# Kernel optimization log

Measured on AMD Instinct MI355X. Metric: run time of the kernel, lower is better.

Reference implementation:

```python
import jax, jax.numpy as jnp
import numpy as np

N, E, T, B = 10000, 80000, 240000, 32
HF, EMB = 256, 64
EDGE_BINS, ANG_BINS = 80, 40
N_CONV = 12  # 4 alignn layers x 2 EGGC + 4 gcn EGGC


def layernorm(x, scale, bias):
    m = x.mean(-1, keepdims=True)
    v = ((x - m) ** 2).mean(-1, keepdims=True)
    return (x - m) / jnp.sqrt(v + 1e-5) * scale + bias


def mlp_layer(x, W, b, ln):
    # Linear -> LayerNorm -> SiLU
    return jax.nn.silu(layernorm(x @ W + b, ln[0], ln[1]))


def rbf(x, vmin, vmax, bins):
    centers = jnp.linspace(vmin, vmax, bins)
    gamma = 0.5 / ((vmax - vmin) / bins) ** 2
    return jnp.exp(-gamma * (x[..., None] - centers) ** 2)


def eggc(W, b, ln_s, ln_b, src, dst, h, e, n_nodes):
    """Edge-gated graph conv. W:[5,F,F] b:[5,F] order: src_gate,dst_gate,edge_gate,src_update,dst_update.
    ln_s/ln_b:[2,F] order: edges, nodes."""
    e_src = h @ W[0] + b[0]
    e_dst = h @ W[1] + b[1]
    sigma = jax.nn.sigmoid(e_src[src] + e_dst[dst] + e @ W[2] + b[2])  # [n_edges, F]
    e_out = layernorm(sigma * e, ln_s[0], ln_b[0])
    Bh = h @ W[4] + b[4]  # dst_update
    sum_sh = jax.ops.segment_sum(Bh[src] * sigma, dst, num_segments=n_nodes)
    sum_s = jax.ops.segment_sum(sigma, dst, num_segments=n_nodes)
    h_out = h @ W[3] + b[3] + sum_sh / (sum_s + 1e-8)  # src_update + gated mean
    return layernorm(h_out, ln_s[1], ln_b[1]), e_out


def setup_inputs() -> dict:
    key = jax.random.key(0)
    ks = jax.random.split(key, 24)
    rn = lambda k, shp: (jax.random.normal(k, shp, dtype=jnp.float32) * 0.05)
    ln_init = lambda f: jnp.stack([jnp.ones((f,), jnp.float32), jnp.zeros((f,), jnp.float32)])
    inp = {
        'atom_features': jax.random.normal(ks[0], (N, 92), dtype=jnp.float32),
        'bondlength': jax.random.uniform(ks[1], (E,), dtype=jnp.float32) * 8.0,
        'angle_h': jax.random.uniform(ks[2], (T,), dtype=jnp.float32) * 2.0 - 1.0,
        'src': jax.random.randint(ks[3], (E,), 0, N, dtype=jnp.int32),
        'dst': jax.random.randint(ks[4], (E,), 0, N, dtype=jnp.int32),
        'lg_src': jax.random.randint(ks[5], (T,), 0, E, dtype=jnp.int32),
        'lg_dst': jax.random.randint(ks[6], (T,), 0, E, dtype=jnp.int32),
        'graph_ids': jnp.sort(jax.random.randint(ks[7], (N,), 0, B)).astype(jnp.int32),
        'atom_W': rn(ks[8], (92, HF)), 'atom_b': jnp.zeros((HF,), jnp.float32), 'atom_ln': ln_init(HF),
        'edge_W1': rn(ks[9], (EDGE_BINS, EMB)), 'edge_b1': jnp.zeros((EMB,), jnp.float32), 'edge_ln1': ln_init(EMB),
        'edge_W2': rn(ks[10], (EMB, HF)), 'edge_b2': jnp.zeros((HF,), jnp.float32), 'edge_ln2': ln_init(HF),
        'ang_W1': rn(ks[11], (ANG_BINS, EMB)), 'ang_b1': jnp.zeros((EMB,), jnp.float32), 'ang_ln1': ln_init(EMB),
        'ang_W2': rn(ks[12], (EMB, HF)), 'ang_b2': jnp.zeros((HF,), jnp.float32), 'ang_ln2': ln_init(HF),
        'conv_W': rn(ks[13], (N_CONV, 5, HF, HF)),
        'conv_b': jnp.zeros((N_CONV, 5, HF), jnp.float32),
        'conv_ln_s': jnp.ones((N_CONV, 2, HF), jnp.float32),
        'conv_ln_b': jnp.zeros((N_CONV, 2, HF), jnp.float32),
    }
    return inp


def reference(atom_features, bondlength, angle_h, src, dst, lg_src, lg_dst, graph_ids,
              atom_W, atom_b, atom_ln, edge_W1, edge_b1, edge_ln1, edge_W2, edge_b2, edge_ln2,
              ang_W1, ang_b1, ang_ln1, ang_W2, ang_b2, ang_ln2,
              conv_W, conv_b, conv_ln_s, conv_ln_b):
    n_nodes = atom_features.shape[0]
    n_edges = bondlength.shape[0]
    # embeddings
    z = mlp_layer(mlp_layer(rbf(angle_h, -1.0, 1.0, ANG_BINS), ang_W1, ang_b1, ang_ln1), ang_W2, ang_b2, ang_ln2)
    x = mlp_layer(atom_features, atom_W, atom_b, atom_ln)
    y = mlp_layer(mlp_layer(rbf(bondlength, 0.0, 8.0, EDGE_BINS), edge_W1, edge_b1, edge_ln1), edge_W2, edge_b2, edge_ln2)
    # 4 ALIGNN layers: edge_update on line graph, then node_update on graph
    for i in range(4):
        j = 2 * i
        y, z = eggc(conv_W[j], conv_b[j], conv_ln_s[j], conv_ln_b[j], lg_src, lg_dst, y, z, n_edges)
        j = 2 * i + 1
        x, y = eggc(conv_W[j], conv_b[j], conv_ln_s[j], conv_ln_b[j], src, dst, x, y, n_nodes)
    # 4 GCN layers
    for i in range(4):
        j = 8 + i
        x, y = eggc(conv_W[j], conv_b[j], conv_ln_s[j], conv_ln_b[j], src, dst, x, y, n_nodes)
    # AvgPooling readout per graph
    sums = jax.ops.segment_sum(x, graph_ids, num_segments=B)
    counts = jax.ops.segment_sum(jnp.ones((n_nodes,), x.dtype), graph_ids, num_segments=B)
    return sums / jnp.maximum(counts, 1.0)[:, None]
```

## Files before the change

### kernel.cpp

```cpp
#include <hip/hip_runtime.h>
#include <hip/hip_bf16.h>

typedef unsigned short u16;
typedef unsigned int u32;
typedef __attribute__((ext_vector_type(8))) short short8;
typedef __attribute__((ext_vector_type(4))) float f32x4;

__device__ __forceinline__ float bf2f(u16 u) { return __uint_as_float(((u32)u) << 16); }
__device__ __forceinline__ u16 f2bf(float f) {
  u32 x = __float_as_uint(f);
  return (u16)((x + 0x7FFFu + ((x >> 16) & 1u)) >> 16);
}
__device__ __forceinline__ void up4(uint2 r, float* o) {
  o[0] = bf2f((u16)(r.x & 0xFFFF)); o[1] = bf2f((u16)(r.x >> 16));
  o[2] = bf2f((u16)(r.y & 0xFFFF)); o[3] = bf2f((u16)(r.y >> 16));
}
__device__ __forceinline__ uint2 pk4(const float* o) {
  uint2 r;
  r.x = (u32)f2bf(o[0]) | ((u32)f2bf(o[1]) << 16);
  r.y = (u32)f2bf(o[2]) | ((u32)f2bf(o[3]) << 16);
  return r;
}
__device__ __forceinline__ float wsum64(float v) {
#pragma unroll
  for (int o = 32; o > 0; o >>= 1) v += __shfl_xor(v, o, 64);
  return v;
}
__device__ __forceinline__ float sigm(float x) { return 1.0f / (1.0f + __expf(-x)); }

__global__ __launch_bounds__(256) void fill_kernel(float* __restrict__ out, int n, float v) {
  int i = blockIdx.x * 256 + threadIdx.x;
  if (i < n) out[i] = v;
}

__global__ __launch_bounds__(256) void wtrans(const float* __restrict__ in,
                                              u16* __restrict__ out, int R, int Ccols) {
  __shared__ float t[64][65];
  const float* ip = in + (size_t)blockIdx.z * R * Ccols;
  u16* op = out + (size_t)blockIdx.z * R * Ccols;
  int kb = blockIdx.x * 64, nb = blockIdx.y * 64;
  int lr = threadIdx.x >> 4, lc = (threadIdx.x & 15) * 4;
#pragma unroll
  for (int p = 0; p < 4; ++p) {
    int k = lr + p * 16;
    float4 v = *(const float4*)(ip + (size_t)(kb + k) * Ccols + nb + lc);
    t[k][lc + 0] = v.x; t[k][lc + 1] = v.y; t[k][lc + 2] = v.z; t[k][lc + 3] = v.w;
  }
  __syncthreads();
#pragma unroll
  for (int p = 0; p < 4; ++p) {
    int n = lr + p * 16;
    uint2 pk;
    pk.x = (u32)f2bf(t[lc + 0][n]) | ((u32)f2bf(t[lc + 1][n]) << 16);
    pk.y = (u32)f2bf(t[lc + 2][n]) | ((u32)f2bf(t[lc + 3][n]) << 16);
    *(uint2*)(op + (size_t)(nb + n) * R + kb + lc) = pk;
  }
}

__global__ __launch_bounds__(256) void csr_hist(const int* __restrict__ dst,
                                                int* __restrict__ hist, int ne) {
  int e = blockIdx.x * 256 + threadIdx.x;
  if (e < ne) atomicAdd(&hist[dst[e]], 1);
}
__global__ __launch_bounds__(1024) void scan1(const int* __restrict__ in,
                                              int* __restrict__ out1, int* __restrict__ bsum, int n) {
  __shared__ int s[1024];
  int i = blockIdx.x * 1024 + threadIdx.x;
  int v = (i < n) ? in[i] : 0;
  s[threadIdx.x] = v; __syncthreads();
  for (int off = 1; off < 1024; off <<= 1) {
    int t = (threadIdx.x >= (u32)off) ? s[threadIdx.x - off] : 0;
    __syncthreads();
    s[threadIdx.x] += t;
    __syncthreads();
  }
  if (i < n) out1[i] = s[threadIdx.x];
  if (threadIdx.x == 1023) bsum[blockIdx.x] = s[1023];
}
__global__ __launch_bounds__(128) void scan2(int* __restrict__ bsum, int nb) {
  __shared__ int s[128];
  int v = (threadIdx.x < (u32)nb) ? bsum[threadIdx.x] : 0;
  s[threadIdx.x] = v; __syncthreads();
  for (int off = 1; off < 128; off <<= 1) {
    int t = (threadIdx.x >= (u32)off) ? s[threadIdx.x - off] : 0;
    __syncthreads();
    s[threadIdx.x] += t;
    __syncthreads();
  }
  if (threadIdx.x < (u32)nb) bsum[threadIdx.x] = threadIdx.x ? s[threadIdx.x - 1] : 0;
}
__global__ __launch_bounds__(256) void scan3(int* __restrict__ offs,
                                             const int* __restrict__ bsum, int n) {
  int i = blockIdx.x * 256 + threadIdx.x;
  if (i == 0) offs[0] = 0;
  if (i < n) offs[1 + i] += bsum[i >> 10];
}
__global__ __launch_bounds__(256) void csr_scatter(const int* __restrict__ dst,
                                                   int* __restrict__ cursor,
                                                   const int* __restrict__ offs,
                                                   int* __restrict__ eid, int ne) {
  int e = blockIdx.x * 256 + threadIdx.x;
  if (e < ne) {
    int d = dst[e];
    int p = offs[d] + atomicAdd(&cursor[d], 1);
    eid[p] = e;
  }
}
__global__ __launch_bounds__(256) void inv_perm(const int* __restrict__ eid,
                                                int* __restrict__ pos, int n) {
  int i = blockIdx.x * 256 + threadIdx.x;
  if (i < n) pos[eid[i]] = i;
}
__global__ __launch_bounds__(256) void remap_k(const int* __restrict__ idx,
                                               const int* __restrict__ map,
                                               int* __restrict__ out, int n) {
  int i = blockIdx.x * 256 + threadIdx.x;
  if (i < n) out[i] = map[idx[i]];
}
__global__ __launch_bounds__(256) void compose_src(const int* __restrict__ eid,
                                                   const int* __restrict__ srcv,
                                                   const int* __restrict__ map,
                                                   int* __restrict__ out, int n) {
  int i = blockIdx.x * 256 + threadIdx.x;
  if (i < n) {
    int s = srcv[eid[i]];
    out[i] = map ? map[s] : s;
  }
}

__global__ __launch_bounds__(256) void embed_s1(
    const float* __restrict__ xin, const float* __restrict__ W1,
    const float* __restrict__ b1, const float* __restrict__ ln1,
    u16* __restrict__ t1, int rows, int bins, float vmin, float vmax,
    const int* __restrict__ perm) {
  int row = (blockIdx.x * 256 + threadIdx.x) >> 6;
  if (row >= rows) return;
  int lane = threadIdx.x & 63;
  float xv = xin[row];
  float rng = vmax - vmin;
  float step = rng / (float)(bins - 1);
  float gamma = 0.5f * ((float)bins / rng) * ((float)bins / rng);
  float rb = 0.f, rb2 = 0.f;
  if (lane < bins) {
    float d = xv - (vmin + lane * step);
    rb = __expf(-gamma * d * d);
  }
  if (bins > 64 && lane < bins - 64) {
    float d = xv - (vmin + (lane + 64) * step);
    rb2 = __expf(-gamma * d * d);
  }
  float u = b1[lane];
  int k1 = bins < 64 ? bins : 64;
  for (int k = 0; k < k1; ++k) {
    float rv = __shfl(rb, k, 64);
    u = fmaf(rv, W1[k * 64 + lane], u);
  }
  for (int k = 64; k < bins; ++k) {
    float rv = __shfl(rb2, k - 64, 64);
    u = fmaf(rv, W1[k * 64 + lane], u);
  }
  float s = wsum64(u), s2 = wsum64(u * u);
  float m = s * (1.f / 64.f), var = s2 * (1.f / 64.f) - m * m;
  float t = (u - m) * rsqrtf(var + 1e-5f) * ln1[lane] + ln1[64 + lane];
  int orow = perm ? perm[row] : row;
  t1[(size_t)orow * 64 + lane] = f2bf(t * sigm(t));
}

__global__ __launch_bounds__(256) void ln_silu(u16* __restrict__ buf,
                                               const float* __restrict__ ln, int rows) {
  int row = (blockIdx.x * 256 + threadIdx.x) >> 6;
  if (row >= rows) return;
  int lane = threadIdx.x & 63;
  int f = lane * 4;
  float v[4];
  up4(*(const uint2*)(buf + (size_t)row * 256 + f), v);
  float s = wsum64(v[0] + v[1] + v[2] + v[3]);
  float s2 = wsum64(v[0] * v[0] + v[1] * v[1] + v[2] * v[2] + v[3] * v[3]);
  float m = s * (1.f / 256.f);
  float rs = rsqrtf(s2 * (1.f / 256.f) - m * m + 1e-5f);
  float o[4];
#pragma unroll
  for (int k = 0; k < 4; ++k) {
    float t = (v[k] - m) * rs * ln[f + k] + ln[256 + f + k];
    o[k] = t * sigm(t);
  }
  *(uint2*)(buf + (size_t)row * 256 + f) = pk4(o);
}

__global__ __launch_bounds__(256) void atom_embed_kernel(
    const float* __restrict__ af, const float* __restrict__ W,
    const float* __restrict__ b, const float* __restrict__ ln,
    u16* __restrict__ out, int rows) {
  int row = blockIdx.x;
  if (row >= rows) return;
  __shared__ float a_s[92];
  __shared__ float red[8];
  int tid = threadIdx.x;
  if (tid < 92) a_s[tid] = af[(size_t)row * 92 + tid];
  __syncthreads();
  float v = b[tid];
#pragma unroll 4
  for (int k = 0; k < 92; ++k) v = fmaf(a_s[k], W[k * 256 + tid], v);
  float s = wsum64(v), s2 = wsum64(v * v);
  int lane = tid & 63, wid = tid >> 6;
  if (lane == 0) { red[wid] = s; red[4 + wid] = s2; }
  __syncthreads();
  s = red[0] + red[1] + red[2] + red[3];
  s2 = red[4] + red[5] + red[6] + red[7];
  float m = s * (1.f / 256.f), var = s2 * (1.f / 256.f) - m * m;
  float t = (v - m) * rsqrtf(var + 1e-5f) * ln[tid] + ln[256 + tid];
  out[(size_t)row * 256 + tid] = f2bf(t * sigm(t));
}

__global__ __launch_bounds__(256) void mfma_gemm(
    const u16* __restrict__ A, const u16* __restrict__ Wt,
    const float* __restrict__ bias, u16* __restrict__ C,
    int M, int K, int ldc, int slab_step) {
  int bm = blockIdx.x * 128;
  if (bm >= M) return;
  int bn = blockIdx.y * 128;
  int slab = (bn >> 8) * slab_step;
  const u16* Wp = Wt + (size_t)slab * 256 * K + (size_t)(bn & 255) * K;
  const float* bp = bias + slab * 256 + (bn & 255);
  int tid = threadIdx.x;
  int w = tid >> 6, lane = tid & 63;
  int q = lane >> 4, r = lane & 15;
  int m0 = (w & 1) * 64;
  int n0 = (w >> 1) * 64;
  const u16* aptr[4];
#pragma unroll
  for (int mi = 0; mi < 4; ++mi) {
    int m = bm + m0 + mi * 16 + r;
    m = m < M - 1 ? m : M - 1;
    aptr[mi] = A + (size_t)m * K + q * 8;
  }
  const u16* wptr[4];
#pragma unroll
  for (int ni = 0; ni < 4; ++ni)
    wptr[ni] = Wp + (size_t)(n0 + ni * 16 + r) * K + q * 8;
  f32x4 acc[4][4] = {};
  for (int kb = 0; kb < K; kb += 32) {
    short8 bfr[4], afr[4];
#pragma unroll
    for (int mi = 0; mi < 4; ++mi) bfr[mi] = *(const short8*)(aptr[mi] + kb);
#pragma unroll
    for (int ni = 0; ni < 4; ++ni) afr[ni] = *(const short8*)(wptr[ni] + kb);
#pragma unroll
    for (int mi = 0; mi < 4; ++mi)
#pragma unroll
      for (int ni = 0; ni < 4; ++ni)
        acc[mi][ni] = __builtin_amdgcn_mfma_f32_16x16x32_bf16(afr[ni], bfr[mi],
                                                              acc[mi][ni], 0, 0, 0);
  }
#pragma unroll
  for (int mi = 0; mi < 4; ++mi) {
    int m = bm + m0 + mi * 16 + r;
    if (m < M) {
#pragma unroll
      for (int ni = 0; ni < 4; ++ni) {
        int n = n0 + ni * 16 + q * 4;
        float4 bv = *(const float4*)(bp + n);
        uint2 o;
        o.x = (u32)f2bf(acc[mi][ni].x + bv.x) | ((u32)f2bf(acc[mi][ni].y + bv.y) << 16);
        o.y = (u32)f2bf(acc[mi][ni].z + bv.z) | ((u32)f2bf(acc[mi][ni].w + bv.w) << 16);
        *(uint2*)(C + (size_t)m * ldc + bn + n) = o;
      }
    }
  }
}

__global__ __launch_bounds__(512) void mega_eggc(
    u16* __restrict__ h, u16* __restrict__ e,
    const u16* __restrict__ G0Bh,
    const u16* __restrict__ Wt13, const float* __restrict__ b13,
    const u16* __restrict__ Wt2, const float* __restrict__ b2v,
    const int* __restrict__ src_perm, const int* __restrict__ offs,
    const float* __restrict__ lnS, const float* __restrict__ lnB, int nn) {
  __shared__ u16 g1ah[16][520];
  __shared__ u16 pe[64][264];
  int tid = threadIdx.x;
  int w = tid >> 6, lane = tid & 63;
  int q = lane >> 4, r = lane & 15;
  int v0 = blockIdx.x * 16;

  {
    int mrow = v0 + r; if (mrow > nn - 1) mrow = nn - 1;
    const u16* arow = h + (size_t)mrow * 256 + q * 8;
    f32x4 acc[4] = {};
    for (int kb = 0; kb < 256; kb += 32) {
      short8 af = *(const short8*)(arow + kb);
#pragma unroll
      for (int t = 0; t < 4; ++t) {
        int ng = (4 * w + t) * 16 + r;
        const u16* wrow = Wt13 + (size_t)(ng >> 8) * 2 * 65536 +
                          (size_t)(ng & 255) * 256 + q * 8;
        short8 wf = *(const short8*)(wrow + kb);
        acc[t] = __builtin_amdgcn_mfma_f32_16x16x32_bf16(wf, af, acc[t], 0, 0, 0);
      }
    }
#pragma unroll
    for (int t = 0; t < 4; ++t) {
      int nb = (4 * w + t) * 16 + q * 4;
      const float* bp = b13 + (nb >> 8) * 2 * 256 + (nb & 255);
      float o[4] = {acc[t].x + bp[0], acc[t].y + bp[1], acc[t].z + bp[2], acc[t].w + bp[3]};
      *(uint2*)&g1ah[r][nb] = pk4(o);
    }
  }
  __syncthreads();

  int f = lane * 4;
  int r0 = offs[v0];
  int vend = v0 + 16 < nn ? v0 + 16 : nn;
  int r1 = offs[vend];
  int vA = v0 + w * 2, vB = vA + 1;
  int eA0 = vA < nn ? offs[vA] : 0, eA1 = vA < nn ? offs[vA + 1] : 0;
  int eB0 = vB < nn ? offs[vB] : 0, eB1 = vB < nn ? offs[vB + 1] : 0;
  float sshA[4] = {0, 0, 0, 0}, ssmA[4] = {0, 0, 0, 0};
  float sshB[4] = {0, 0, 0, 0}, ssmB[4] = {0, 0, 0, 0};
  float lwe[4], lbe[4];
#pragma unroll
  for (int k = 0; k < 4; ++k) { lwe[k] = lnS[f + k]; lbe[k] = lnB[f + k]; }

  for (int ec = r0; ec < r1; ec += 64) {
    {
      const u16* w0p = Wt2 + (size_t)((2 * w) * 16 + r) * 256 + q * 8;
      const u16* w1p = Wt2 + (size_t)((2 * w + 1) * 16 + r) * 256 + q * 8;
      f32x4 acc[4][2] = {};
      for (int kb = 0; kb < 256; kb += 32) {
        short8 wf0 = *(const short8*)(w0p + kb);
        short8 wf1 = *(const short8*)(w1p + kb);
#pragma unroll
        for (int mt = 0; mt < 4; ++mt) {
          int erow = ec + mt * 16 + r;
          if (erow > r1 - 1) erow = r1 - 1;
          short8 af = *(const short8*)(e + (size_t)erow * 256 + kb + q * 8);
          acc[mt][0] = __builtin_amdgcn_mfma_f32_16x16x32_bf16(wf0, af, acc[mt][0], 0, 0, 0);
          acc[mt][1] = __builtin_amdgcn_mfma_f32_16x16x32_bf16(wf1, af, acc[mt][1], 0, 0, 0);
        }
      }
#pragma unroll
      for (int mt = 0; mt < 4; ++mt)
#pragma unroll
        for (int nt = 0; nt < 2; ++nt) {
          int nb = (2 * w + nt) * 16 + q * 4;
          float o[4] = {acc[mt][nt].x + b2v[nb], acc[mt][nt].y + b2v[nb + 1],
                        acc[mt][nt].z + b2v[nb + 2], acc[mt][nt].w + b2v[nb + 3]};
          *(uint2*)&pe[mt * 16 + r][nb] = pk4(o);
        }
    }
    __syncthreads();
    int ce = ec + 64 < r1 ? ec + 64 : r1;
#pragma unroll
    for (int jj = 0; jj < 2; ++jj) {
      int vv = jj ? vB : vA;
      int i0 = jj ? eB0 : eA0, i1 = jj ? eB1 : eA1;
      int lo = i0 > ec ? i0 : ec, hi = i1 < ce ? i1 : ce;
      for (int i = lo; i < hi; ++i) {
        int sv = src_perm[i];
        float g0[4], bh[4], pv[4], ev[4], g1v[4];
        up4(*(const uint2*)(G0Bh + (size_t)sv * 512 + f), g0);
        up4(*(const uint2*)(G0Bh + (size_t)sv * 512 + 256 + f), bh);
        up4(*(const uint2*)&pe[i - ec][f], pv);
        up4(*(const uint2*)(e + (size_t)i * 256 + f), ev);
        up4(*(const uint2*)&g1ah[vv - v0][f], g1v);
        float t[4];
        float ssum = 0.f, s2sum = 0.f;
#pragma unroll
        for (int k = 0; k < 4; ++k) {
          float sg = sigm(g0[k] + g1v[k] + pv[k]);
          t[k] = sg * ev[k];
          if (jj) { sshB[k] = fmaf(bh[k], sg, sshB[k]); ssmB[k] += sg; }
          else    { sshA[k] = fmaf(bh[k], sg, sshA[k]); ssmA[k] += sg; }
          ssum += t[k]; s2sum += t[k] * t[k];
        }
        float s1 = wsum64(ssum), s2 = wsum64(s2sum);
        float mn = s1 * (1.f / 256.f);
        float rs = rsqrtf(s2 * (1.f / 256.f) - mn * mn + 1e-5f);
        float o[4];
#pragma unroll
        for (int k = 0; k < 4; ++k) o[k] = (t[k] - mn) * rs * lwe[k] + lbe[k];
        *(uint2*)(e + (size_t)i * 256 + f) = pk4(o);
      }
    }
    __syncthreads();
  }
#pragma unroll
  for (int jj = 0; jj < 2; ++jj) {
    int vv = jj ? vB : vA;
    if (vv < nn) {
      float ah[4], tt[4];
      up4(*(const uint2*)&g1ah[vv - v0][256 + f], ah);
      float ssum = 0.f, s2sum = 0.f;
#pragma unroll
      for (int k = 0; k < 4; ++k) {
        float sh = jj ? sshB[k] : sshA[k];
        float sm = jj ? ssmB[k] : ssmA[k];
        tt[k] = ah[k] + sh / (sm + 1e-8f);
        ssum += tt[k]; s2sum += tt[k] * tt[k];
      }
      float s1 = wsum64(ssum), s2 = wsum64(s2sum);
      float mn = s1 * (1.f / 256.f);
      float rs = rsqrtf(s2 * (1.f / 256.f) - mn * mn + 1e-5f);
      float o[4];
#pragma unroll
      for (int k = 0; k < 4; ++k)
        o[k] = (tt[k] - mn) * rs * lnS[256 + f + k] + lnB[256 + f + k];
      *(uint2*)(h + (size_t)vv * 256 + f) = pk4(o);
    }
  }
}

__global__ __launch_bounds__(256) void pool_acc(
    const u16* __restrict__ x, const int* __restrict__ gid,
    float* __restrict__ out, float* __restrict__ cnt, int n) {
  int v = (blockIdx.x * 256 + threadIdx.x) >> 6;
  if (v >= n) return;
  int lane = threadIdx.x & 63;
  int f = lane * 4;
  int g = gid[v];
  float xv[4];
  up4(*(const uint2*)(x + (size_t)v * 256 + f), xv);
  float* p = out + (size_t)g * 256 + f;
  unsafeAtomicAdd(p + 0, xv[0]);
  unsafeAtomicAdd(p + 1, xv[1]);
  unsafeAtomicAdd(p + 2, xv[2]);
  unsafeAtomicAdd(p + 3, xv[3]);
  if (lane == 0) unsafeAtomicAdd(cnt + g, 1.0f);
}
__global__ __launch_bounds__(256) void pool_div(float* __restrict__ out,
                                                const float* __restrict__ cnt, int n) {
  int i = blockIdx.x * blockDim.x + threadIdx.x;
  if (i < n) out[i] /= fmaxf(cnt[i >> 8], 1.0f);
}

extern "C" void kernel_launch(void* const* d_in, const int* in_sizes, int n_in,
                              void* d_out, int out_size, void* d_ws, size_t ws_size,
                              hipStream_t stream) {
  const float* atom_features = (const float*)d_in[0];
  const float* bondlength    = (const float*)d_in[1];
  const float* angle_h       = (const float*)d_in[2];
  const int*   src           = (const int*)d_in[3];
  const int*   dst           = (const int*)d_in[4];
  const int*   lg_src        = (const int*)d_in[5];
  const int*   lg_dst        = (const int*)d_in[6];
  const int*   gid           = (const int*)d_in[7];
  const float* atom_W  = (const float*)d_in[8];
  const float* atom_b  = (const float*)d_in[9];
  const float* atom_ln = (const float*)d_in[10];
  const float* edge_W1 = (const float*)d_in[11];
  const float* edge_b1 = (const float*)d_in[12];
  const float* edge_ln1= (const float*)d_in[13];
  const float* edge_W2 = (const float*)d_in[14];
  const float* edge_b2 = (const float*)d_in[15];
  const float* edge_ln2= (const float*)d_in[16];
  const float* ang_W1  = (const float*)d_in[17];
  const float* ang_b1  = (const float*)d_in[18];
  const float* ang_ln1 = (const float*)d_in[19];
  const float* ang_W2  = (const float*)d_in[20];
  const float* ang_b2  = (const float*)d_in[21];
  const float* ang_ln2 = (const float*)d_in[22];
  const float* conv_W  = (const float*)d_in[23];
  const float* conv_b  = (const float*)d_in[24];
  const float* conv_lns= (const float*)d_in[25];
  const float* conv_lnb= (const float*)d_in[26];

  int N = in_sizes[0] / 92;
  int E = in_sizes[1];
  int T = in_sizes[2];

  char* ws = (char*)d_ws;
  size_t o = 0;
  auto alloc = [&](size_t bytes) { size_t r = o; o = (o + bytes + 255) & ~(size_t)255; return r; };
  u16* z     = (u16*)(ws + alloc((size_t)T * 512));
  u16* y     = (u16*)(ws + alloc((size_t)E * 512));
  u16* x     = (u16*)(ws + alloc((size_t)N * 512));
  int* offsL = (int*)(ws + alloc((size_t)(E + 1) * 4));
  int* offsA = (int*)(ws + alloc((size_t)(N + 1) * 4));
  int* spL   = (int*)(ws + alloc((size_t)T * 4));
  int* spA   = (int*)(ws + alloc((size_t)E * 4));
  int* pA    = (int*)(ws + alloc((size_t)E * 4));
  int* pL    = (int*)(ws + alloc((size_t)T * 4));
  int* eidL  = (int*)(ws + alloc((size_t)T * 4));
  int* eidA  = (int*)(ws + alloc((size_t)E * 4));
  int* ldSt  = (int*)(ws + alloc((size_t)T * 4));
  int* tmp   = (int*)(ws + alloc((size_t)(E > N ? E : N) * 4));
  int* bsum  = (int*)(ws + alloc(1024));
  float* cnt = (float*)(ws + alloc(1024));
  u16* WtAll = (u16*)(ws + alloc((size_t)12 * 5 * 65536 * 2));
  u16* WtAng = (u16*)(ws + alloc((size_t)16384 * 2));
  u16* WtEdg = (u16*)(ws + alloc((size_t)16384 * 2));
  size_t scratch_base = o;
  size_t need = scratch_base + (size_t)E * 1024;
  {
    size_t embed_need = scratch_base + ((size_t)T + E) * 128;
    if (embed_need > need) need = embed_need;
  }
  if (ws_size < need) {
    fill_kernel<<<(out_size + 255) / 256, 256, 0, stream>>>(
        (float*)d_out, out_size, (float)(ws_size >> 20));
    return;
  }

  wtrans<<<dim3(4, 4, 60), 256, 0, stream>>>(conv_W, WtAll, 256, 256);
  wtrans<<<dim3(1, 4, 1), 256, 0, stream>>>(ang_W2, WtAng, 64, 256);
  wtrans<<<dim3(1, 4, 1), 256, 0, stream>>>(edge_W2, WtEdg, 64, 256);

  auto build_csr = [&](const int* dvec, int ne_, int nn_, int* offs_, int* eid_) {
    hipMemsetAsync(tmp, 0, (size_t)nn_ * 4, stream);
    csr_hist<<<(ne_ + 255) / 256, 256, 0, stream>>>(dvec, tmp, ne_);
    int nb = (nn_ + 1023) / 1024;
    scan1<<<nb, 1024, 0, stream>>>(tmp, offs_ + 1, bsum, nn_);
    scan2<<<1, 128, 0, stream>>>(bsum, nb);
    scan3<<<(nn_ + 255) / 256, 256, 0, stream>>>(offs_, bsum, nn_);
    hipMemsetAsync(tmp, 0, (size_t)nn_ * 4, stream);
    csr_scatter<<<(ne_ + 255) / 256, 256, 0, stream>>>(dvec, tmp, offs_, eid_, ne_);
  };
  build_csr(dst, E, N, offsA, eidA);
  inv_perm<<<(E + 255) / 256, 256, 0, stream>>>(eidA, pA, E);
  compose_src<<<(E + 255) / 256, 256, 0, stream>>>(eidA, src, nullptr, spA, E);
  remap_k<<<(T + 255) / 256, 256, 0, stream>>>(lg_dst, pA, ldSt, T);
  build_csr(ldSt, T, E, offsL, eidL);
  inv_perm<<<(T + 255) / 256, 256, 0, stream>>>(eidL, pL, T);
  compose_src<<<(T + 255) / 256, 256, 0, stream>>>(eidL, lg_src, pA, spL, T);

  u16* t1T = (u16*)(ws + scratch_base);
  u16* t1E = t1T + (size_t)T * 64;
  embed_s1<<<(T + 3) / 4, 256, 0, stream>>>(angle_h, ang_W1, ang_b1, ang_ln1,
                                            t1T, T, 40, -1.f, 1.f, pL);
  embed_s1<<<(E + 3) / 4, 256, 0, stream>>>(bondlength, edge_W1, edge_b1, edge_ln1,
                                            t1E, E, 80, 0.f, 8.f, pA);
  mfma_gemm<<<dim3((T + 127) / 128, 2), 256, 0, stream>>>(
      t1T, WtAng, ang_b2, z, T, 64, 256, 1);
  mfma_gemm<<<dim3((E + 127) / 128, 2), 256, 0, stream>>>(
      t1E, WtEdg, edge_b2, y, E, 64, 256, 1);
  ln_silu<<<(T + 3) / 4, 256, 0, stream>>>(z, ang_ln2, T);
  ln_silu<<<(E + 3) / 4, 256, 0, stream>>>(y, edge_ln2, E);
  atom_embed_kernel<<<N, 256, 0, stream>>>(atom_features, atom_W, atom_b, atom_ln, x, N);

  u16* G0Bh = (u16*)(ws + scratch_base);
  for (int l = 0; l < 12; ++l) {
    const u16* WtL  = WtAll + (size_t)l * 5 * 65536;
    const float* bl = conv_b + (size_t)l * 5 * 256;
    const float* lnS = conv_lns + (size_t)l * 512;
    const float* lnB = conv_lnb + (size_t)l * 512;
    bool line = (l < 8) && ((l & 1) == 0);
    u16* h = line ? y : x;
    u16* e = line ? z : y;
    const int* sperm = line ? spL : spA;
    const int* offs  = line ? offsL : offsA;
    int nn = line ? E : N;

    mfma_gemm<<<dim3((nn + 127) / 128, 4), 256, 0, stream>>>(
        h, WtL, bl, G0Bh, nn, 256, 512, 4);
    mega_eggc<<<(nn + 15) / 16, 512, 0, stream>>>(
        h, e, G0Bh, WtL + 65536, bl + 256, WtL + 2 * 65536, bl + 2 * 256,
        sperm, offs, lnS, lnB, nn);
  }

  hipMemsetAsync(d_out, 0, (size_t)out_size * sizeof(float), stream);
  hipMemsetAsync(cnt, 0, 256 * sizeof(float), stream);
  pool_acc<<<(N + 3) / 4, 256, 0, stream>>>(x, gid, (float*)d_out, cnt, N);
  pool_div<<<(out_size + 255) / 256, 256, 0, stream>>>((float*)d_out, cnt, out_size);
}
```

Before: 5.469 ms.

## Split EGGC kernel into line/atom variants with prefetched edge gathers

For atom-graph layers, all four node-side projections are computed in one wider GEMM through a slab map, so the fused kernel no longer recomputes the dst-gate and src-update MFMA per block. Both fused kernels now cache CSR offsets in shared memory and load each node's gate row into registers once. The per-edge loop interleaves the two nodes a wave owns and prefetches the next edge's gathered rows to hide memory latency. The cost is more register pressure, and a larger scratch write for the atom layers.

```diff
diff --git a/kernel.cpp b/kernel.cpp
--- a/kernel.cpp
+++ b/kernel.cpp
@@ -215,11 +215,11 @@
 __global__ __launch_bounds__(256) void mfma_gemm(
     const u16* __restrict__ A, const u16* __restrict__ Wt,
     const float* __restrict__ bias, u16* __restrict__ C,
-    int M, int K, int ldc, int slab_step) {
+    int M, int K, int ldc, u32 smap) {
   int bm = blockIdx.x * 128;
   if (bm >= M) return;
   int bn = blockIdx.y * 128;
-  int slab = (bn >> 8) * slab_step;
+  int slab = (smap >> ((bn >> 8) * 8)) & 0xFF;
   const u16* Wp = Wt + (size_t)slab * 256 * K + (size_t)(bn & 255) * K;
   const float* bp = bias + slab * 256 + (bn & 255);
   int tid = threadIdx.x;
@@ -269,20 +269,20 @@
   }
 }
 
-__global__ __launch_bounds__(512) void mega_eggc(
-    u16* __restrict__ h, u16* __restrict__ e,
-    const u16* __restrict__ G0Bh,
+__global__ __launch_bounds__(512) void mega_line(
+    u16* __restrict__ h, u16* __restrict__ e, const u16* __restrict__ G0Bh,
     const u16* __restrict__ Wt13, const float* __restrict__ b13,
     const u16* __restrict__ Wt2, const float* __restrict__ b2v,
     const int* __restrict__ src_perm, const int* __restrict__ offs,
     const float* __restrict__ lnS, const float* __restrict__ lnB, int nn) {
   __shared__ u16 g1ah[16][520];
   __shared__ u16 pe[64][264];
+  __shared__ int oloc[17];
   int tid = threadIdx.x;
   int w = tid >> 6, lane = tid & 63;
   int q = lane >> 4, r = lane & 15;
   int v0 = blockIdx.x * 16;
-
+  if (tid < 17) { int v = v0 + tid; oloc[tid] = offs[v < nn ? v : nn]; }
   {
     int mrow = v0 + r; if (mrow > nn - 1) mrow = nn - 1;
     const u16* arow = h + (size_t)mrow * 256 + q * 8;
@@ -307,19 +307,17 @@
     }
   }
   __syncthreads();
-
   int f = lane * 4;
-  int r0 = offs[v0];
-  int vend = v0 + 16 < nn ? v0 + 16 : nn;
-  int r1 = offs[vend];
-  int vA = v0 + w * 2, vB = vA + 1;
-  int eA0 = vA < nn ? offs[vA] : 0, eA1 = vA < nn ? offs[vA + 1] : 0;
-  int eB0 = vB < nn ? offs[vB] : 0, eB1 = vB < nn ? offs[vB + 1] : 0;
-  float sshA[4] = {0, 0, 0, 0}, ssmA[4] = {0, 0, 0, 0};
-  float sshB[4] = {0, 0, 0, 0}, ssmB[4] = {0, 0, 0, 0};
+  int r0 = oloc[0], r1 = oloc[16];
+  int eA0 = oloc[2 * w], eA1 = oloc[2 * w + 1];
+  int eB0 = oloc[2 * w + 1], eB1 = oloc[2 * w + 2];
+  float sshA[4] = {}, ssmA[4] = {}, sshB[4] = {}, ssmB[4] = {};
   float lwe[4], lbe[4];
 #pragma unroll
   for (int k = 0; k < 4; ++k) { lwe[k] = lnS[f + k]; lbe[k] = lnB[f + k]; }
+  float g1A[4], g1Bv[4];
+  up4(*(const uint2*)&g1ah[2 * w][f], g1A);
+  up4(*(const uint2*)&g1ah[2 * w + 1][f], g1Bv);
 
   for (int ec = r0; ec < r1; ec += 64) {
     {
@@ -349,47 +347,255 @@
         }
     }
     __syncthreads();
-    int ce = ec + 64 < r1 ? ec + 64 : r1;
-#pragma unroll
-    for (int jj = 0; jj < 2; ++jj) {
-      int vv = jj ? vB : vA;
-      int i0 = jj ? eB0 : eA0, i1 = jj ? eB1 : eA1;
-      int lo = i0 > ec ? i0 : ec, hi = i1 < ce ? i1 : ce;
-      for (int i = lo; i < hi; ++i) {
-        int sv = src_perm[i];
-        float g0[4], bh[4], pv[4], ev[4], g1v[4];
-        up4(*(const uint2*)(G0Bh + (size_t)sv * 512 + f), g0);
-        up4(*(const uint2*)(G0Bh + (size_t)sv * 512 + 256 + f), bh);
-        up4(*(const uint2*)&pe[i - ec][f], pv);
-        up4(*(const uint2*)(e + (size_t)i * 256 + f), ev);
-        up4(*(const uint2*)&g1ah[vv - v0][f], g1v);
-        float t[4];
-        float ssum = 0.f, s2sum = 0.f;
-#pragma unroll
-        for (int k = 0; k < 4; ++k) {
-          float sg = sigm(g0[k] + g1v[k] + pv[k]);
-          t[k] = sg * ev[k];
-          if (jj) { sshB[k] = fmaf(bh[k], sg, sshB[k]); ssmB[k] += sg; }
-          else    { sshA[k] = fmaf(bh[k], sg, sshA[k]); ssmA[k] += sg; }
-          ssum += t[k]; s2sum += t[k] * t[k];
-        }
-        float s1 = wsum64(ssum), s2 = wsum64(s2sum);
-        float mn = s1 * (1.f / 256.f);
-        float rs = rsqrtf(s2 * (1.f / 256.f) - mn * mn + 1e-5f);
-        float o[4];
-#pragma unroll
-        for (int k = 0; k < 4; ++k) o[k] = (t[k] - mn) * rs * lwe[k] + lbe[k];
-        *(uint2*)(e + (size_t)i * 256 + f) = pk4(o);
+    {
+      int ce = ec + 64 < r1 ? ec + 64 : r1;
+      int ia = eA0 > ec ? eA0 : ec, iaE = eA1 < ce ? eA1 : ce;
+      int ib = eB0 > ec ? eB0 : ec, ibE = eB1 < ce ? eB1 : ce;
+      uint2 ag0, abh, aev, bg0, bbh, bev;
+      if (ia < iaE) {
+        int sv = src_perm[ia];
+        ag0 = *(const uint2*)(G0Bh + (size_t)sv * 512 + f);
+        abh = *(const uint2*)(G0Bh + (size_t)sv * 512 + 256 + f);
+        aev = *(const uint2*)(e + (size_t)ia * 256 + f);
+      }
+      if (ib < ibE) {
+        int sv = src_perm[ib];
+        bg0 = *(const uint2*)(G0Bh + (size_t)sv * 512 + f);
+        bbh = *(const uint2*)(G0Bh + (size_t)sv * 512 + 256 + f);
+        bev = *(const uint2*)(e + (size_t)ib * 256 + f);
+      }
+      while (ia < iaE || ib < ibE) {
+        uint2 nag0, nabh, naev, nbg0, nbbh, nbev;
+        if (ia + 1 < iaE) {
+          int sv = src_perm[ia + 1];
+          nag0 = *(const uint2*)(G0Bh + (size_t)sv * 512 + f);
+          nabh = *(const uint2*)(G0Bh + (size_t)sv * 512 + 256 + f);
+          naev = *(const uint2*)(e + (size_t)(ia + 1) * 256 + f);
+        }
+        if (ib + 1 < ibE) {
+          int sv = src_perm[ib + 1];
+          nbg0 = *(const uint2*)(G0Bh + (size_t)sv * 512 + f);
+          nbbh = *(const uint2*)(G0Bh + (size_t)sv * 512 + 256 + f);
+          nbev = *(const uint2*)(e + (size_t)(ib + 1) * 256 + f);
+        }
+        if (ia < iaE) {
+          float g0v[4], bhv[4], pv[4], ev[4], t[4];
+          up4(ag0, g0v); up4(abh, bhv); up4(aev, ev);
+          up4(*(const uint2*)&pe[ia - ec][f], pv);
+          float ssum = 0.f, s2sum = 0.f;
+#pragma unroll
+          for (int k = 0; k < 4; ++k) {
+            float sg = sigm(g0v[k] + g1A[k] + pv[k]);
+            t[k] = sg * ev[k];
+            sshA[k] = fmaf(bhv[k], sg, sshA[k]);
+            ssmA[k] += sg;
+            ssum += t[k]; s2sum += t[k] * t[k];
+          }
+          float s1 = wsum64(ssum), s2 = wsum64(s2sum);
+          float mn = s1 * (1.f / 256.f);
+          float rs = rsqrtf(s2 * (1.f / 256.f) - mn * mn + 1e-5f);
+          float o[4];
+#pragma unroll
+          for (int k = 0; k < 4; ++k) o[k] = (t[k] - mn) * rs * lwe[k] + lbe[k];
+          *(uint2*)(e + (size_t)ia * 256 + f) = pk4(o);
+        }
+        if (ib < ibE) {
+          float g0v[4], bhv[4], pv[4], ev[4], t[4];
+          up4(bg0, g0v); up4(bbh, bhv); up4(bev, ev);
+          up4(*(const uint2*)&pe[ib - ec][f], pv);
+          float ssum = 0.f, s2sum = 0.f;
+#pragma unroll
+          for (int k = 0; k < 4; ++k) {
+            float sg = sigm(g0v[k] + g1Bv[k] + pv[k]);
+            t[k] = sg * ev[k];
+            sshB[k] = fmaf(bhv[k], sg, sshB[k]);
+            ssmB[k] += sg;
+            ssum += t[k]; s2sum += t[k] * t[k];
+          }
+          float s1 = wsum64(ssum), s2 = wsum64(s2sum);
+          float mn = s1 * (1.f / 256.f);
+          float rs = rsqrtf(s2 * (1.f / 256.f) - mn * mn + 1e-5f);
+          float o[4];
+#pragma unroll
+          for (int k = 0; k < 4; ++k) o[k] = (t[k] - mn) * rs * lwe[k] + lbe[k];
+          *(uint2*)(e + (size_t)ib * 256 + f) = pk4(o);
+        }
+        ag0 = nag0; abh = nabh; aev = naev;
+        bg0 = nbg0; bbh = nbbh; bev = nbev;
+        ia += (ia < iaE) ? 1 : 0;
+        ib += (ib < ibE) ? 1 : 0;
       }
     }
     __syncthreads();
   }
 #pragma unroll
   for (int jj = 0; jj < 2; ++jj) {
-    int vv = jj ? vB : vA;
+    int vv = v0 + 2 * w + jj;
     if (vv < nn) {
       float ah[4], tt[4];
-      up4(*(const uint2*)&g1ah[vv - v0][256 + f], ah);
+      up4(*(const uint2*)&g1ah[2 * w + jj][256 + f], ah);
+      float ssum = 0.f, s2sum = 0.f;
+#pragma unroll
+      for (int k = 0; k < 4; ++k) {
+        float sh = jj ? sshB[k] : sshA[k];
+        float sm = jj ? ssmB[k] : ssmA[k];
+        tt[k] = ah[k] + sh / (sm + 1e-8f);
+        ssum += tt[k]; s2sum += tt[k] * tt[k];
+      }
+      float s1 = wsum64(ssum), s2 = wsum64(s2sum);
+      float mn = s1 * (1.f / 256.f);
+      float rs = rsqrtf(s2 * (1.f / 256.f) - mn * mn + 1e-5f);
+      float o[4];
+#pragma unroll
+      for (int k = 0; k < 4; ++k)
+        o[k] = (tt[k] - mn) * rs * lnS[256 + f + k] + lnB[256 + f + k];
+      *(uint2*)(h + (size_t)vv * 256 + f) = pk4(o);
+    }
+  }
+}
+
+__global__ __launch_bounds__(512) void mega_atom(
+    u16* __restrict__ h, u16* __restrict__ e, const u16* __restrict__ GAll,
+    const u16* __restrict__ Wt2, const float* __restrict__ b2v,
+    const int* __restrict__ src_perm, const int* __restrict__ offs,
+    const float* __restrict__ lnS, const float* __restrict__ lnB, int nn) {
+  __shared__ u16 pe[64][264];
+  __shared__ int oloc[17];
+  int tid = threadIdx.x;
+  int w = tid >> 6, lane = tid & 63;
+  int q = lane >> 4, r = lane & 15;
+  int v0 = blockIdx.x * 16;
+  if (tid < 17) { int v = v0 + tid; oloc[tid] = offs[v < nn ? v : nn]; }
+  __syncthreads();
+  int f = lane * 4;
+  int r0 = oloc[0], r1 = oloc[16];
+  int eA0 = oloc[2 * w], eA1 = oloc[2 * w + 1];
+  int eB0 = oloc[2 * w + 1], eB1 = oloc[2 * w + 2];
+  float sshA[4] = {}, ssmA[4] = {}, sshB[4] = {}, ssmB[4] = {};
+  float lwe[4], lbe[4];
+#pragma unroll
+  for (int k = 0; k < 4; ++k) { lwe[k] = lnS[f + k]; lbe[k] = lnB[f + k]; }
+  int vAc = v0 + 2 * w;     if (vAc > nn - 1) vAc = nn - 1;
+  int vBc = v0 + 2 * w + 1; if (vBc > nn - 1) vBc = nn - 1;
+  float g1A[4], g1Bv[4];
+  up4(*(const uint2*)(GAll + (size_t)vAc * 1024 + 256 + f), g1A);
+  up4(*(const uint2*)(GAll + (size_t)vBc * 1024 + 256 + f), g1Bv);
+
+  for (int ec = r0; ec < r1; ec += 64) {
+    {
+      const u16* w0p = Wt2 + (size_t)((2 * w) * 16 + r) * 256 + q * 8;
+      const u16* w1p = Wt2 + (size_t)((2 * w + 1) * 16 + r) * 256 + q * 8;
+      f32x4 acc[4][2] = {};
+      for (int kb = 0; kb < 256; kb += 32) {
+        short8 wf0 = *(const short8*)(w0p + kb);
+        short8 wf1 = *(const short8*)(w1p + kb);
+#pragma unroll
+        for (int mt = 0; mt < 4; ++mt) {
+          int erow = ec + mt * 16 + r;
+          if (erow > r1 - 1) erow = r1 - 1;
+          short8 af = *(const short8*)(e + (size_t)erow * 256 + kb + q * 8);
+          acc[mt][0] = __builtin_amdgcn_mfma_f32_16x16x32_bf16(wf0, af, acc[mt][0], 0, 0, 0);
+          acc[mt][1] = __builtin_amdgcn_mfma_f32_16x16x32_bf16(wf1, af, acc[mt][1], 0, 0, 0);
+        }
+      }
+#pragma unroll
+      for (int mt = 0; mt < 4; ++mt)
+#pragma unroll
+        for (int nt = 0; nt < 2; ++nt) {
+          int nb = (2 * w + nt) * 16 + q * 4;
+          float o[4] = {acc[mt][nt].x + b2v[nb], acc[mt][nt].y + b2v[nb + 1],
+                        acc[mt][nt].z + b2v[nb + 2], acc[mt][nt].w + b2v[nb + 3]};
+          *(uint2*)&pe[mt * 16 + r][nb] = pk4(o);
+        }
+    }
+    __syncthreads();
+    {
+      int ce = ec + 64 < r1 ? ec + 64 : r1;
+      int ia = eA0 > ec ? eA0 : ec, iaE = eA1 < ce ? eA1 : ce;
+      int ib = eB0 > ec ? eB0 : ec, ibE = eB1 < ce ? eB1 : ce;
+      uint2 ag0, abh, aev, bg0, bbh, bev;
+      if (ia < iaE) {
+        int sv = src_perm[ia];
+        ag0 = *(const uint2*)(GAll + (size_t)sv * 1024 + f);
+        abh = *(const uint2*)(GAll + (size_t)sv * 1024 + 768 + f);
+        aev = *(const uint2*)(e + (size_t)ia * 256 + f);
+      }
+      if (ib < ibE) {
+        int sv = src_perm[ib];
+        bg0 = *(const uint2*)(GAll + (size_t)sv * 1024 + f);
+        bbh = *(const uint2*)(GAll + (size_t)sv * 1024 + 768 + f);
+        bev = *(const uint2*)(e + (size_t)ib * 256 + f);
+      }
+      while (ia < iaE || ib < ibE) {
+        uint2 nag0, nabh, naev, nbg0, nbbh, nbev;
+        if (ia + 1 < iaE) {
+          int sv = src_perm[ia + 1];
+          nag0 = *(const uint2*)(GAll + (size_t)sv * 1024 + f);
+          nabh = *(const uint2*)(GAll + (size_t)sv * 1024 + 768 + f);
+          naev = *(const uint2*)(e + (size_t)(ia + 1) * 256 + f);
+        }
+        if (ib + 1 < ibE) {
+          int sv = src_perm[ib + 1];
+          nbg0 = *(const uint2*)(GAll + (size_t)sv * 1024 + f);
+          nbbh = *(const uint2*)(GAll + (size_t)sv * 1024 + 768 + f);
+          nbev = *(const uint2*)(e + (size_t)(ib + 1) * 256 + f);
+        }
+        if (ia < iaE) {
+          float g0v[4], bhv[4], pv[4], ev[4], t[4];
+          up4(ag0, g0v); up4(abh, bhv); up4(aev, ev);
+          up4(*(const uint2*)&pe[ia - ec][f], pv);
+          float ssum = 0.f, s2sum = 0.f;
+#pragma unroll
+          for (int k = 0; k < 4; ++k) {
+            float sg = sigm(g0v[k] + g1A[k] + pv[k]);
+            t[k] = sg * ev[k];
+            sshA[k] = fmaf(bhv[k], sg, sshA[k]);
+            ssmA[k] += sg;
+            ssum += t[k]; s2sum += t[k] * t[k];
+          }
+          float s1 = wsum64(ssum), s2 = wsum64(s2sum);
+          float mn = s1 * (1.f / 256.f);
+          float rs = rsqrtf(s2 * (1.f / 256.f) - mn * mn + 1e-5f);
+          float o[4];
+#pragma unroll
+          for (int k = 0; k < 4; ++k) o[k] = (t[k] - mn) * rs * lwe[k] + lbe[k];
+          *(uint2*)(e + (size_t)ia * 256 + f) = pk4(o);
+        }
+        if (ib < ibE) {
+          float g0v[4], bhv[4], pv[4], ev[4], t[4];
+          up4(bg0, g0v); up4(bbh, bhv); up4(bev, ev);
+          up4(*(const uint2*)&pe[ib - ec][f], pv);
+          float ssum = 0.f, s2sum = 0.f;
+#pragma unroll
+          for (int k = 0; k < 4; ++k) {
+            float sg = sigm(g0v[k] + g1Bv[k] + pv[k]);
+            t[k] = sg * ev[k];
+            sshB[k] = fmaf(bhv[k], sg, sshB[k]);
+            ssmB[k] += sg;
+            ssum += t[k]; s2sum += t[k] * t[k];
+          }
+          float s1 = wsum64(ssum), s2 = wsum64(s2sum);
+          float mn = s1 * (1.f / 256.f);
+          float rs = rsqrtf(s2 * (1.f / 256.f) - mn * mn + 1e-5f);
+          float o[4];
+#pragma unroll
+          for (int k = 0; k < 4; ++k) o[k] = (t[k] - mn) * rs * lwe[k] + lbe[k];
+          *(uint2*)(e + (size_t)ib * 256 + f) = pk4(o);
+        }
+        ag0 = nag0; abh = nabh; aev = naev;
+        bg0 = nbg0; bbh = nbbh; bev = nbev;
+        ia += (ia < iaE) ? 1 : 0;
+        ib += (ib < ibE) ? 1 : 0;
+      }
+    }
+    __syncthreads();
+  }
+#pragma unroll
+  for (int jj = 0; jj < 2; ++jj) {
+    int vv = v0 + 2 * w + jj;
+    if (vv < nn) {
+      float ah[4], tt[4];
+      up4(*(const uint2*)(GAll + (size_t)vv * 1024 + 512 + f), ah);
       float ssum = 0.f, s2sum = 0.f;
 #pragma unroll
       for (int k = 0; k < 4; ++k) {
@@ -530,31 +736,34 @@
   embed_s1<<<(E + 3) / 4, 256, 0, stream>>>(bondlength, edge_W1, edge_b1, edge_ln1,
                                             t1E, E, 80, 0.f, 8.f, pA);
   mfma_gemm<<<dim3((T + 127) / 128, 2), 256, 0, stream>>>(
-      t1T, WtAng, ang_b2, z, T, 64, 256, 1);
+      t1T, WtAng, ang_b2, z, T, 64, 256, 0u);
   mfma_gemm<<<dim3((E + 127) / 128, 2), 256, 0, stream>>>(
-      t1E, WtEdg, edge_b2, y, E, 64, 256, 1);
+      t1E, WtEdg, edge_b2, y, E, 64, 256, 0u);
   ln_silu<<<(T + 3) / 4, 256, 0, stream>>>(z, ang_ln2, T);
   ln_silu<<<(E + 3) / 4, 256, 0, stream>>>(y, edge_ln2, E);
   atom_embed_kernel<<<N, 256, 0, stream>>>(atom_features, atom_W, atom_b, atom_ln, x, N);
 
-  u16* G0Bh = (u16*)(ws + scratch_base);
   for (int l = 0; l < 12; ++l) {
     const u16* WtL  = WtAll + (size_t)l * 5 * 65536;
     const float* bl = conv_b + (size_t)l * 5 * 256;
     const float* lnS = conv_lns + (size_t)l * 512;
     const float* lnB = conv_lnb + (size_t)l * 512;
     bool line = (l < 8) && ((l & 1) == 0);
-    u16* h = line ? y : x;
-    u16* e = line ? z : y;
-    const int* sperm = line ? spL : spA;
-    const int* offs  = line ? offsL : offsA;
-    int nn = line ? E : N;
-
-    mfma_gemm<<<dim3((nn + 127) / 128, 4), 256, 0, stream>>>(
-        h, WtL, bl, G0Bh, nn, 256, 512, 4);
-    mega_eggc<<<(nn + 15) / 16, 512, 0, stream>>>(
-        h, e, G0Bh, WtL + 65536, bl + 256, WtL + 2 * 65536, bl + 2 * 256,
-        sperm, offs, lnS, lnB, nn);
+    if (line) {
+      u16* G0Bh = (u16*)(ws + scratch_base);
+      mfma_gemm<<<dim3((E + 127) / 128, 4), 256, 0, stream>>>(
+          y, WtL, bl, G0Bh, E, 256, 512, 0u | (4u << 8));
+      mega_line<<<(E + 15) / 16, 512, 0, stream>>>(
+          y, z, G0Bh, WtL + 65536, bl + 256, WtL + 2 * 65536, bl + 2 * 256,
+          spL, offsL, lnS, lnB, E);
+    } else {
+      u16* GAll = (u16*)(ws + scratch_base);
+      mfma_gemm<<<dim3((N + 127) / 128, 8), 256, 0, stream>>>(
+          x, WtL, bl, GAll, N, 256, 1024, 0u | (1u << 8) | (3u << 16) | (4u << 24));
+      mega_atom<<<(N + 15) / 16, 512, 0, stream>>>(
+          x, y, GAll, WtL + 2 * 65536, bl + 2 * 256,
+          spA, offsA, lnS, lnB, N);
+    }
   }
 
   hipMemsetAsync(d_out, 0, (size_t)out_size * sizeof(float), stream);
```

Result: slower. 5.649 ms (+3.3%).
